# Kernel optimization log

Measured on AMD Instinct MI355X. Metric: run time of the kernel, lower is better.

## Reference

```python
import jax, jax.numpy as jnp
import numpy as np

B, C, L = 32, 8, 2048
K, S = 512, 64  # num_shapelets, shapelets_size


def setup_inputs() -> dict:
    key = jax.random.key(0)
    k1, k2 = jax.random.split(key)
    x = jax.random.normal(k1, (B, C, L), dtype=jnp.float32)
    shapelets = jax.random.normal(k2, (C, K, S), dtype=jnp.float32)
    return {"x": x, "shapelets": shapelets}


def reference(x, shapelets):
    # x: [B, C, L]; shapelets: [C, K, S]
    s = shapelets.shape[-1]
    n_dims = x.shape[1]
    W = x.shape[2] - s + 1  # number of sliding windows
    # unfold(2, S, 1): gather overlapping windows -> [B, C, W, S]
    idx = jnp.arange(W)[:, None] + jnp.arange(s)[None, :]
    xw = x[:, :, idx]
    # L2-normalize windows along window length (clamp min like torch)
    xw = xw / jnp.maximum(jnp.linalg.norm(xw, axis=-1, keepdims=True), 1e-8)
    # L2-normalize shapelets along length
    sn = shapelets / jnp.maximum(jnp.linalg.norm(shapelets, axis=-1, keepdims=True), 1e-8)
    # matmul [B,C,W,S] @ [C,S,K] then sum over C, fused into one einsum -> [B, W, K]
    sim = jnp.einsum('bcws,cks->bwk', xw, sn) / n_dims
    sim = jax.nn.relu(sim)
    # max over window positions -> [B, K]; keep the singleton channel dim like torch ([B,1,K])
    out = jnp.max(sim, axis=1)
    return out[:, None, :]
```

## Files before the change

### kernel.cpp

```cpp
#include <hip/hip_runtime.h>


#define B_ 32
#define C_ 8
#define L_ 2048
#define K_ 512
#define S_ 64
#define W_ 1985
#define XS_ 2176

typedef _Float16 f16x8  __attribute__((ext_vector_type(8)));
typedef _Float16 f16x8u __attribute__((ext_vector_type(8), aligned(4)));
typedef float    f32x16 __attribute__((ext_vector_type(16)));

__global__ __launch_bounds__(256)
void prep_k(const float* __restrict__ x, const float* __restrict__ sh,
            _Float16* __restrict__ Bp, float* __restrict__ invn,
            _Float16* __restrict__ xh0, _Float16* __restrict__ xh1,
            float* __restrict__ out) {
    __shared__ float xr[L_];
    const int tid = threadIdx.x;
    const int blk = blockIdx.x;

    if (blk < 128) {
        const int sb   = blk * 4 + (tid >> 6);
        const int c    = sb >> 6;
        const int kq   = (sb >> 4) & 3;
        const int nt   = sb & 15;
        const int lane = tid & 63;
        const int half = lane >> 5;
        const int q    = nt * 32 + (lane & 31);

        const float4* sp = (const float4*)(sh + (size_t)(c * K_ + q) * S_);
        float ss = 0.f;
        #pragma unroll
        for (int i = 0; i < 8; ++i) {
            float4 v = sp[half * 8 + i];
            ss += v.x * v.x + v.y * v.y + v.z * v.z + v.w * v.w;
        }
        ss += __shfl_xor(ss, 32);
        float inv = 1.f / fmaxf(sqrtf(ss), 1e-8f);

        float4 u0 = sp[kq * 4 + half * 2];
        float4 u1 = sp[kq * 4 + half * 2 + 1];
        f16x8 o;
        o[0] = (_Float16)(u0.x * inv); o[1] = (_Float16)(u0.y * inv);
        o[2] = (_Float16)(u0.z * inv); o[3] = (_Float16)(u0.w * inv);
        o[4] = (_Float16)(u1.x * inv); o[5] = (_Float16)(u1.y * inv);
        o[6] = (_Float16)(u1.z * inv); o[7] = (_Float16)(u1.w * inv);
        ((f16x8*)Bp)[((c * 4 + kq) * 16 + nt) * 64 + lane] = o;
    } else {
        const int r = blk - 128;
        const float* xp = x + (size_t)r * L_;
        for (int i = tid; i < L_ / 4; i += 256)
            ((float4*)xr)[i] = ((const float4*)xp)[i];
        __syncthreads();

        float* ivp = invn + (size_t)r * L_;
        const int w0 = tid * 8;
        float ss = 0.f;
        if (w0 < W_) {
            #pragma unroll
            for (int j = 0; j < S_; ++j) { float v = xr[w0 + j]; ss += v * v; }
        }
        #pragma unroll
        for (int u = 0; u < 8; ++u) {
            int w = w0 + u;
            float o = 0.f;
            if (u > 0 && w < W_)
                ss += xr[w + 63] * xr[w + 63] - xr[w - 1] * xr[w - 1];
            if (w < W_) o = 0.125f / fmaxf(sqrtf(ss), 1e-8f);
            if (w < L_) ivp[w] = o;
        }

        _Float16* p0 = xh0 + (size_t)r * XS_;
        _Float16* p1 = xh1 + (size_t)r * XS_;
        for (int i = tid; i < XS_ / 8; i += 256) {
            f16x8 o0, o1;
            #pragma unroll
            for (int j = 0; j < 8; ++j) {
                int e = i * 8 + j;
                o0[j] = (_Float16)((e     < L_) ? xr[e]     : 0.f);
                o1[j] = (_Float16)((e + 1 < L_) ? xr[e + 1] : 0.f);
            }
            ((f16x8*)p0)[i] = o0;
            ((f16x8*)p1)[i] = o1;
        }
        if (r < 64) out[r * 256 + tid] = 0.f;
    }
}

__device__ __forceinline__ void glds16(const void* g, void* l) {
    __builtin_amdgcn_global_load_lds(
        (const __attribute__((address_space(1))) unsigned int*)g,
        (__attribute__((address_space(3))) unsigned int*)l, 16, 0, 0);
}

__device__ __forceinline__ void loadA(
    int c, const _Float16* __restrict__ xbase, const float* __restrict__ ivbase,
    int m0, int m1, f16x8 (&ar)[8], float (&iv)[2])
{
    iv[0] = ivbase[(size_t)c * L_ + m0];
    iv[1] = ivbase[(size_t)c * L_ + m1];
    const _Float16* xp = xbase + (size_t)c * XS_;
    #pragma unroll
    for (int mt = 0; mt < 2; ++mt)
        #pragma unroll
        for (int ks = 0; ks < 4; ++ks)
            ar[mt * 4 + ks] = *(const f16x8u*)(xp + mt * 32 + ks * 16);
}

__device__ __forceinline__ void compC(
    int c, const f16x8* __restrict__ bsl, int lane,
    const f16x8 (&ar)[8], const float (&iv)[2], f32x16 (&acc)[2][2])
{
    f16x8 bf[8];
    #pragma unroll
    for (int ks = 0; ks < 4; ++ks)
        #pragma unroll
        for (int nt = 0; nt < 2; ++nt)
            bf[ks * 2 + nt] = bsl[(c * 8 + ks * 2 + nt) * 64 + lane];

    const _Float16 h0 = (_Float16)iv[0], h1 = (_Float16)iv[1];
    f16x8 is0, is1;
    #pragma unroll
    for (int j = 0; j < 8; ++j) { is0[j] = h0; is1[j] = h1; }

    __builtin_amdgcn_s_setprio(1);
    #pragma unroll
    for (int ks = 0; ks < 4; ++ks) {
        f16x8 a0 = ar[0 * 4 + ks] * is0;
        f16x8 a1 = ar[1 * 4 + ks] * is1;
        #pragma unroll
        for (int nt = 0; nt < 2; ++nt) {
            acc[0][nt] = __builtin_amdgcn_mfma_f32_32x32x16_f16(
                a0, bf[ks * 2 + nt], acc[0][nt], 0, 0, 0);
            acc[1][nt] = __builtin_amdgcn_mfma_f32_32x32x16_f16(
                a1, bf[ks * 2 + nt], acc[1][nt], 0, 0, 0);
        }
    }
    __builtin_amdgcn_s_setprio(0);
}

__global__ __launch_bounds__(256, 2)
void mcs_k(const _Float16* __restrict__ xh0, const _Float16* __restrict__ xh1,
           const _Float16* __restrict__ Bp, const float* __restrict__ invn,
           float* __restrict__ out) {
    const int wt  = blockIdx.x;
    const int ng  = blockIdx.y;
    const int b   = blockIdx.z;
    const int tid = threadIdx.x;
    const int lane = tid & 63;
    const int wv   = tid >> 6;

    const int l31 = lane & 31;
    const int lh  = lane >> 5;
    const int Wb  = wt * 256 + wv * 64;
    const int m0  = Wb + l31;
    const int m1  = Wb + 32 + l31;

    __shared__ f16x8 Bs[64][64];

    {
        const f16x8* bp = (const f16x8*)Bp;
        #pragma unroll
        for (int u = 0; u < 16; ++u) {
            const int e   = wv * 16 + u;
            const int c   = e >> 3;
            const int sub = e & 7;
            const int src = ((c * 4 + (sub >> 1)) * 16 + ng * 2 + (sub & 1)) * 64;
            glds16(bp + src + lane, &Bs[e][0]);
        }
    }

    const _Float16* xb = (l31 & 1) ? (xh1 - 1) : xh0;
    const _Float16* xbase = xb + (size_t)b * C_ * XS_ + Wb + l31 + lh * 8;
    const float*   ivbase = invn + (size_t)b * C_ * L_;

    f32x16 acc[2][2];
    #pragma unroll
    for (int mt = 0; mt < 2; ++mt)
        #pragma unroll
        for (int nt = 0; nt < 2; ++nt)
            #pragma unroll
            for (int r = 0; r < 16; ++r) acc[mt][nt][r] = 0.f;

    f16x8 aA[8], aB[8];
    float ivA[2], ivB[2];

    loadA(0, xbase, ivbase, m0, m1, aA, ivA);
    __syncthreads();

    #pragma unroll 1
    for (int cp = 0; cp < 4; ++cp) {
        const int c0 = cp * 2;
        loadA(c0 + 1, xbase, ivbase, m0, m1, aB, ivB);
        compC(c0, &Bs[0][0], lane, aA, ivA, acc);
        if (cp < 3)
            loadA(c0 + 2, xbase, ivbase, m0, m1, aA, ivA);
        compC(c0 + 1, &Bs[0][0], lane, aB, ivB, acc);
    }

    #pragma unroll
    for (int nt = 0; nt < 2; ++nt) {
        float v = 0.f;
        #pragma unroll
        for (int mt = 0; mt < 2; ++mt)
            #pragma unroll
            for (int r = 0; r < 16; ++r) v = fmaxf(v, acc[mt][nt][r]);
        v = fmaxf(v, __shfl_xor(v, 32));
        if (lane < 32)
            atomicMax((unsigned int*)(out + (size_t)b * K_ + ng * 64 + nt * 32 + l31),
                      __float_as_uint(v));
    }
}

extern "C" void kernel_launch(void* const* d_in, const int* in_sizes, int n_in,
                              void* d_out, int out_size, void* d_ws, size_t ws_size,
                              hipStream_t stream) {
    const float* x  = (const float*)d_in[0];
    const float* sh = (const float*)d_in[1];
    float* out = (float*)d_out;

    _Float16* Bp   = (_Float16*)d_ws;
    float*    invn = (float*)((char*)d_ws + (512 << 10));
    _Float16* xh0  = (_Float16*)((char*)d_ws + (512 << 10) + (2 << 20));
    _Float16* xh1  = xh0 + (size_t)B_ * C_ * XS_;

    prep_k<<<dim3(384), dim3(256), 0, stream>>>(x, sh, Bp, invn, xh0, xh1, out);
    mcs_k<<<dim3(8, 8, B_), dim3(256), 0, stream>>>(xh0, xh1, Bp, invn, out);
}
```

Before: 98.81 us.

## Widen N tile to 128 shapelets per block with two-phase staged B loads

Result: faster. 94.74 us (-4.1%).

```diff
diff --git a/kernel.cpp b/kernel.cpp
--- a/kernel.cpp
+++ b/kernel.cpp
@@ -98,48 +98,38 @@
 
 __device__ __forceinline__ void loadA(
     int c, const _Float16* __restrict__ xbase, const float* __restrict__ ivbase,
-    int m0, int m1, f16x8 (&ar)[8], float (&iv)[2])
+    int m0, int m1, f16x8 (&g)[6], float (&iv)[2])
 {
     iv[0] = ivbase[(size_t)c * L_ + m0];
     iv[1] = ivbase[(size_t)c * L_ + m1];
     const _Float16* xp = xbase + (size_t)c * XS_;
     #pragma unroll
-    for (int mt = 0; mt < 2; ++mt)
-        #pragma unroll
-        for (int ks = 0; ks < 4; ++ks)
-            ar[mt * 4 + ks] = *(const f16x8u*)(xp + mt * 32 + ks * 16);
+    for (int p = 0; p < 6; ++p)
+        g[p] = *(const f16x8u*)(xp + p * 16);
 }
 
 __device__ __forceinline__ void compC(
-    int c, const f16x8* __restrict__ bsl, int lane,
-    const f16x8 (&ar)[8], const float (&iv)[2], f32x16 (&acc)[2][2])
+    int cc, const f16x8* __restrict__ Bsl, int lane,
+    const f16x8 (&g)[6], const float (&iv)[2], f32x16 (&acc)[2][4])
 {
-    f16x8 bf[8];
-    #pragma unroll
-    for (int ks = 0; ks < 4; ++ks)
-        #pragma unroll
-        for (int nt = 0; nt < 2; ++nt)
-            bf[ks * 2 + nt] = bsl[(c * 8 + ks * 2 + nt) * 64 + lane];
-
     const _Float16 h0 = (_Float16)iv[0], h1 = (_Float16)iv[1];
     f16x8 is0, is1;
     #pragma unroll
     for (int j = 0; j < 8; ++j) { is0[j] = h0; is1[j] = h1; }
 
-    __builtin_amdgcn_s_setprio(1);
     #pragma unroll
     for (int ks = 0; ks < 4; ++ks) {
-        f16x8 a0 = ar[0 * 4 + ks] * is0;
-        f16x8 a1 = ar[1 * 4 + ks] * is1;
-        #pragma unroll
-        for (int nt = 0; nt < 2; ++nt) {
+        f16x8 a0 = g[ks]     * is0;
+        f16x8 a1 = g[ks + 2] * is1;
+        #pragma unroll
+        for (int nt = 0; nt < 4; ++nt) {
+            f16x8 bf = Bsl[((cc * 4 + ks) * 4 + nt) * 64 + lane];
             acc[0][nt] = __builtin_amdgcn_mfma_f32_32x32x16_f16(
-                a0, bf[ks * 2 + nt], acc[0][nt], 0, 0, 0);
+                a0, bf, acc[0][nt], 0, 0, 0);
             acc[1][nt] = __builtin_amdgcn_mfma_f32_32x32x16_f16(
-                a1, bf[ks * 2 + nt], acc[1][nt], 0, 0, 0);
-        }
-    }
-    __builtin_amdgcn_s_setprio(0);
+                a1, bf, acc[1][nt], 0, 0, 0);
+        }
+    }
 }
 
 __global__ __launch_bounds__(256, 2)
@@ -159,50 +149,55 @@
     const int m0  = Wb + l31;
     const int m1  = Wb + 32 + l31;
 
-    __shared__ f16x8 Bs[64][64];
-
-    {
-        const f16x8* bp = (const f16x8*)Bp;
-        #pragma unroll
-        for (int u = 0; u < 16; ++u) {
-            const int e   = wv * 16 + u;
-            const int c   = e >> 3;
-            const int sub = e & 7;
-            const int src = ((c * 4 + (sub >> 1)) * 16 + ng * 2 + (sub & 1)) * 64;
-            glds16(bp + src + lane, &Bs[e][0]);
-        }
-    }
+    __shared__ __attribute__((aligned(16))) f16x8 Bs[64][64];
 
     const _Float16* xb = (l31 & 1) ? (xh1 - 1) : xh0;
     const _Float16* xbase = xb + (size_t)b * C_ * XS_ + Wb + l31 + lh * 8;
     const float*   ivbase = invn + (size_t)b * C_ * L_;
-
-    f32x16 acc[2][2];
+    const f16x8*   Bsl = &Bs[0][0];
+    const f16x8*   bp  = (const f16x8*)Bp;
+
+    f32x16 acc[2][4];
     #pragma unroll
     for (int mt = 0; mt < 2; ++mt)
         #pragma unroll
-        for (int nt = 0; nt < 2; ++nt)
+        for (int nt = 0; nt < 4; ++nt)
             #pragma unroll
             for (int r = 0; r < 16; ++r) acc[mt][nt][r] = 0.f;
 
-    f16x8 aA[8], aB[8];
-    float ivA[2], ivB[2];
-
-    loadA(0, xbase, ivbase, m0, m1, aA, ivA);
-    __syncthreads();
+    f16x8 gE[6], gO[6];
+    float ivE[2], ivO[2];
+
+    #define STAGE(p)                                                    \
+        { _Pragma("unroll")                                             \
+          for (int u = 0; u < 16; ++u) {                                \
+              const int e  = wv * 16 + u;                               \
+              const int cc = e >> 4, ks = (e >> 2) & 3, nt = e & 3;     \
+              const int src = ((((p) * 4 + cc) * 4 + ks) * 16           \
+                               + ng * 4 + nt) * 64;                     \
+              glds16(bp + src + lane, &Bs[e][0]);                       \
+          } }
 
     #pragma unroll 1
-    for (int cp = 0; cp < 4; ++cp) {
-        const int c0 = cp * 2;
-        loadA(c0 + 1, xbase, ivbase, m0, m1, aB, ivB);
-        compC(c0, &Bs[0][0], lane, aA, ivA, acc);
-        if (cp < 3)
-            loadA(c0 + 2, xbase, ivbase, m0, m1, aA, ivA);
-        compC(c0 + 1, &Bs[0][0], lane, aB, ivB, acc);
-    }
-
-    #pragma unroll
-    for (int nt = 0; nt < 2; ++nt) {
+    for (int p = 0; p < 2; ++p) {
+        const int c0 = p * 4;
+        if (p) __syncthreads();
+        STAGE(p);
+        loadA(c0 + 0, xbase, ivbase, m0, m1, gE, ivE);
+        loadA(c0 + 1, xbase, ivbase, m0, m1, gO, ivO);
+        __syncthreads();
+
+        compC(0, Bsl, lane, gE, ivE, acc);
+        loadA(c0 + 2, xbase, ivbase, m0, m1, gE, ivE);
+        compC(1, Bsl, lane, gO, ivO, acc);
+        loadA(c0 + 3, xbase, ivbase, m0, m1, gO, ivO);
+        compC(2, Bsl, lane, gE, ivE, acc);
+        compC(3, Bsl, lane, gO, ivO, acc);
+    }
+    #undef STAGE
+
+    #pragma unroll
+    for (int nt = 0; nt < 4; ++nt) {
         float v = 0.f;
         #pragma unroll
         for (int mt = 0; mt < 2; ++mt)
@@ -210,7 +205,7 @@
             for (int r = 0; r < 16; ++r) v = fmaxf(v, acc[mt][nt][r]);
         v = fmaxf(v, __shfl_xor(v, 32));
         if (lane < 32)
-            atomicMax((unsigned int*)(out + (size_t)b * K_ + ng * 64 + nt * 32 + l31),
+            atomicMax((unsigned int*)(out + (size_t)b * K_ + ng * 128 + nt * 32 + l31),
                       __float_as_uint(v));
     }
 }
@@ -228,5 +223,5 @@
     _Float16* xh1  = xh0 + (size_t)B_ * C_ * XS_;
 
     prep_k<<<dim3(384), dim3(256), 0, stream>>>(x, sh, Bp, invn, xh0, xh1, out);
-    mcs_k<<<dim3(8, 8, B_), dim3(256), 0, stream>>>(xh0, xh1, Bp, invn, out);
-}
+    mcs_k<<<dim3(8, 4, B_), dim3(256), 0, stream>>>(xh0, xh1, Bp, invn, out);
+}
```
